# Optimization experiments

Measured on AMD Instinct MI355X. Metric: run time of the kernel, lower is better.

## Reference

```python
import jax, jax.numpy as jnp
import numpy as np

M = 8      # window size
S = 4      # shift size
NH = 3     # num heads
EPS = 1e-5


def _rel_pos_index(m):
    coords = np.stack(np.meshgrid(np.arange(m), np.arange(m), indexing='ij')).reshape(2, -1)
    rel = (coords[:, :, None] - coords[:, None, :]).transpose(1, 2, 0)
    rel[:, :, 0] += m - 1
    rel[:, :, 1] += m - 1
    rel[:, :, 0] *= 2 * m - 1
    return rel.sum(-1)  # [m^2, m^2]


def _attn_mask(Hs, Ws, m, s):
    img = np.zeros((Hs, Ws))
    cnt = 0
    for hsl in (slice(0, -m), slice(-m, -s), slice(-s, None)):
        for wsl in (slice(0, -m), slice(-m, -s), slice(-s, None)):
            img[hsl, wsl] = cnt
            cnt += 1
    mw = img.reshape(Hs // m, m, Ws // m, m).transpose(0, 2, 1, 3).reshape(-1, m * m)
    d = mw[:, None, :] - mw[:, :, None]
    return np.where(d != 0, -100.0, 0.0).astype(np.float32)  # [nW, N, N]


def _ln(x, w, b):
    mu = jnp.mean(x, -1, keepdims=True)
    var = jnp.mean(jnp.square(x - mu), -1, keepdims=True)
    return (x - mu) * jax.lax.rsqrt(var + EPS) * w + b


def setup_inputs() -> dict:
    key = jax.random.key(0)
    ks = jax.random.split(key, 8)
    B, Hs, Ws, C = 16, 128, 128, 96
    MLPH = 4 * C
    inp = {
        'x': jax.random.normal(ks[0], (B, Hs * Ws, C), jnp.float32),
        'norm1_w': jnp.ones((C,), jnp.float32),
        'norm1_b': jnp.zeros((C,), jnp.float32),
        'qkv_w': jax.random.normal(ks[1], (C, 3 * C), jnp.float32) * 0.02,
        'qkv_b': jnp.zeros((3 * C,), jnp.float32),
        'rpb_table': jax.random.normal(ks[2], ((2 * M - 1) ** 2, NH), jnp.float32) * 0.02,
        'proj_w': jax.random.normal(ks[3], (C, C), jnp.float32) * 0.02,
        'proj_b': jnp.zeros((C,), jnp.float32),
        'norm2_w': jnp.ones((C,), jnp.float32),
        'norm2_b': jnp.zeros((C,), jnp.float32),
        'mlp_w1': jax.random.normal(ks[4], (C, MLPH), jnp.float32) * 0.02,
        'mlp_b1': jnp.zeros((MLPH,), jnp.float32),
        'mlp_w2': jax.random.normal(ks[5], (MLPH, C), jnp.float32) * 0.02,
        'mlp_b2': jnp.zeros((C,), jnp.float32),
        'H': Hs,
        'W': Ws,
    }
    return inp


def reference(x, norm1_w, norm1_b, qkv_w, qkv_b, rpb_table, proj_w, proj_b,
              norm2_w, norm2_b, mlp_w1, mlp_b1, mlp_w2, mlp_b2, H, W):
    B, L, C = x.shape
    N = M * M
    HD = C // NH
    scale = HD ** -0.5
    nW = (H // M) * (W // M)

    rpi = jnp.asarray(_rel_pos_index(M))                    # [N, N]
    mask = jnp.asarray(_attn_mask(H, W, M, S))              # [nW, N, N]

    shortcut = x
    h = _ln(x, norm1_w, norm1_b).reshape(B, H, W, C)
    h = jnp.roll(h, (-S, -S), axis=(1, 2))
    # window partition -> [B, nW, N, C]
    h = h.reshape(B, H // M, M, W // M, M, C).transpose(0, 1, 3, 2, 4, 5)
    h = h.reshape(B, nW, N, C)

    qkv = (h @ qkv_w + qkv_b).reshape(B, nW, N, 3, NH, HD)
    q, k, v = qkv[..., 0, :, :], qkv[..., 1, :, :], qkv[..., 2, :, :]  # [B,nW,N,NH,HD]
    attn = jnp.einsum('bwnhd,bwmhd->bwhnm', q, k) * scale              # [B,nW,NH,N,N]
    rp_bias = rpb_table[rpi].transpose(2, 0, 1)                        # [NH,N,N]
    attn = attn + rp_bias[None, None] + mask[None, :, None]
    attn = jax.nn.softmax(attn, axis=-1)
    out = jnp.einsum('bwhnm,bwmhd->bwnhd', attn, v).reshape(B, nW, N, C)
    out = out @ proj_w + proj_b

    # window reverse -> [B, H, W, C]
    out = out.reshape(B, H // M, W // M, M, M, C).transpose(0, 1, 3, 2, 4, 5)
    out = out.reshape(B, H, W, C)
    out = jnp.roll(out, (S, S), axis=(1, 2)).reshape(B, L, C)

    x1 = shortcut + out
    h2 = _ln(x1, norm2_w, norm2_b)
    h2 = jax.nn.gelu(h2 @ mlp_w1 + mlp_b1, approximate=False) @ mlp_w2 + mlp_b2
    return x1 + h2
```

## Files before the change

### kernel.cpp

```cpp
#include <hip/hip_runtime.h>
#include <hip/hip_bf16.h>

typedef __hip_bfloat16 hbf16;
typedef __bf16 bf16_t;
typedef __bf16 bf16x4 __attribute__((ext_vector_type(4)));
typedef __bf16 bf16x8 __attribute__((ext_vector_type(8)));
typedef float  f32x4  __attribute__((ext_vector_type(4)));

__device__ __forceinline__ float b2f(hbf16 v) { return __bfloat162float(v); }

template<bool F32>
__device__ __forceinline__ float ld(const void* p, size_t i) {
    return F32 ? ((const float*)p)[i] : b2f(((const hbf16*)p)[i]);
}

constexpr int Hh  = 128, Ww = 128, Cc = 96;
constexpr int MM  = 8, SS = 4, NHh = 3, C3 = 288;
constexpr int MLPH = 384;
constexpr int NWH = Hh / MM;
constexpr int NW  = NWH * NWH;
constexpr float SCALE = 0.17677669529663687f;
constexpr float EPSf  = 1e-5f;

constexpr int WQKV_ELEMS = C3 * Cc;
constexpr int WP_ELEMS   = Cc * Cc;
constexpr int W1_ELEMS   = MLPH * Cc;
constexpr int W2_ELEMS   = Cc * MLPH;
constexpr int W_TOTAL    = WQKV_ELEMS + WP_ELEMS + W1_ELEMS + W2_ELEMS;

constexpr int OFF_A   = 0;
constexpr int OFF_KA  = 6144;
constexpr int OFF_VT  = 12288;
constexpr int SMEM_E  = 18432;

__global__ void prep_w(const void* __restrict__ qkvw, const void* __restrict__ pw,
                       const void* __restrict__ w1,   const void* __restrict__ w2,
                       const void* __restrict__ n1w,  bf16_t* __restrict__ ws)
{
    const bool f32 = (((const unsigned*)n1w)[0] == 0x3F800000u);
    int i = blockIdx.x * 256 + threadIdx.x;
    if (i < WQKV_ELEMS) {
        int j = i / Cc, k = i - j * Cc;
        ws[i] = (bf16_t)(f32 ? ((const float*)qkvw)[(size_t)k * C3 + j]
                             : b2f(((const hbf16*)qkvw)[(size_t)k * C3 + j]));
    } else if (i < WQKV_ELEMS + WP_ELEMS) {
        int t = i - WQKV_ELEMS;
        int n = t / Cc, r0 = t - n * Cc;
        int p = r0 >> 5, r2 = r0 & 31;
        int quad = r2 >> 3, ii = r2 & 7;
        int k = p * 32 + ((ii >> 2) << 4) + quad * 4 + (ii & 3);
        ws[i] = (bf16_t)(f32 ? ((const float*)pw)[(size_t)k * Cc + n]
                             : b2f(((const hbf16*)pw)[(size_t)k * Cc + n]));
    } else if (i < WQKV_ELEMS + WP_ELEMS + W1_ELEMS) {
        int t = i - WQKV_ELEMS - WP_ELEMS;
        int j = t / Cc, k = t - j * Cc;
        ws[i] = (bf16_t)(f32 ? ((const float*)w1)[(size_t)k * MLPH + j]
                             : b2f(((const hbf16*)w1)[(size_t)k * MLPH + j]));
    } else if (i < W_TOTAL) {
        int t = i - WQKV_ELEMS - WP_ELEMS - W1_ELEMS;
        int n = t / MLPH, r0 = t - n * MLPH;
        int p = r0 >> 5, r2 = r0 & 31;
        int quad = r2 >> 3, ii = r2 & 7;
        int k = p * 32 + ((ii >> 2) << 4) + quad * 4 + (ii & 3);
        ws[i] = (bf16_t)(f32 ? ((const float*)w2)[(size_t)k * Cc + n]
                             : b2f(((const hbf16*)w2)[(size_t)k * Cc + n]));
    }
}

template<bool F32>
__device__ __forceinline__ void swin_body(
    bf16_t* __restrict__ sm,
    const void* __restrict__ x,
    const void* __restrict__ n1w, const void* __restrict__ n1b,
    const void* __restrict__ qkvb, const void* __restrict__ rpb,
    const void* __restrict__ pb,
    const void* __restrict__ n2w, const void* __restrict__ n2b,
    const void* __restrict__ b1,  const void* __restrict__ b2,
    const bf16_t* __restrict__ wq_t, const bf16_t* __restrict__ wp_f,
    const bf16_t* __restrict__ w1_t, const bf16_t* __restrict__ w2_f,
    float* __restrict__ out)
{
    const int tid  = threadIdx.x;
    const int lane = tid & 63;
    const int wv   = tid >> 6;
    const int c16  = lane & 15;
    const int quad = lane >> 4;
    const int b    = blockIdx.x / NW;
    const int w    = blockIdx.x % NW;
    const int wi   = w / NWH, wj = w % NWH;

    {
        const int t = tid >> 2, q = tid & 3;
        const int ri = wi * MM + (t >> 3), rj = wj * MM + (t & 7);
        const int gi = (ri + SS) & (Hh - 1), gj = (rj + SS) & (Ww - 1);
        const size_t base = ((size_t)((b * Hh + gi) * Ww + gj)) * Cc + q * 24;
        float v[24]; float s = 0.f, s2 = 0.f;
        if (F32) {
            const float* xf = (const float*)x + base;
            #pragma unroll
            for (int i = 0; i < 6; ++i) {
                float4 t4 = *(const float4*)(xf + i * 4);
                v[i*4+0] = t4.x; v[i*4+1] = t4.y; v[i*4+2] = t4.z; v[i*4+3] = t4.w;
            }
        } else {
            #pragma unroll
            for (int i = 0; i < 24; ++i) v[i] = b2f(((const hbf16*)x)[base + i]);
        }
        #pragma unroll
        for (int i = 0; i < 24; ++i) { s += v[i]; s2 += v[i] * v[i]; }
        s  += __shfl_xor(s, 1);  s  += __shfl_xor(s, 2);
        s2 += __shfl_xor(s2, 1); s2 += __shfl_xor(s2, 2);
        const float mu = s / Cc, var = s2 / Cc - mu * mu, rstd = rsqrtf(var + EPSf);
        #pragma unroll
        for (int ch = 0; ch < 3; ++ch) {
            float wv8[8], bv8[8];
            if (F32) {
                const float* wf = (const float*)n1w + q * 24 + ch * 8;
                const float* bf = (const float*)n1b + q * 24 + ch * 8;
                float4 w0 = *(const float4*)wf, w1q = *(const float4*)(wf + 4);
                float4 b0 = *(const float4*)bf, b1q = *(const float4*)(bf + 4);
                wv8[0]=w0.x; wv8[1]=w0.y; wv8[2]=w0.z; wv8[3]=w0.w;
                wv8[4]=w1q.x; wv8[5]=w1q.y; wv8[6]=w1q.z; wv8[7]=w1q.w;
                bv8[0]=b0.x; bv8[1]=b0.y; bv8[2]=b0.z; bv8[3]=b0.w;
                bv8[4]=b1q.x; bv8[5]=b1q.y; bv8[6]=b1q.z; bv8[7]=b1q.w;
            } else {
                #pragma unroll
                for (int i = 0; i < 8; ++i) {
                    int cidx = q * 24 + ch * 8 + i;
                    wv8[i] = b2f(((const hbf16*)n1w)[cidx]);
                    bv8[i] = b2f(((const hbf16*)n1b)[cidx]);
                }
            }
            bf16x8 pk;
            #pragma unroll
            for (int i = 0; i < 8; ++i)
                pk[i] = (bf16_t)((v[ch * 8 + i] - mu) * rstd * wv8[i] + bv8[i]);
            *(bf16x8*)&sm[OFF_A + ((q * 3 + ch) * 64 + t) * 8] = pk;
        }
    }

    {
        bf16x8 ha[3];
        #pragma unroll
        for (int ks = 0; ks < 3; ++ks)
            ha[ks] = *(const bf16x8*)&sm[OFF_A + ((ks * 4 + quad) * 64 + wv * 16 + c16) * 8];
        for (int nt = 0; nt < 18; ++nt) {
            const int j = nt * 16 + c16;
            const bf16_t* wrow = wq_t + (size_t)j * Cc + quad * 8;
            f32x4 acc = {0.f, 0.f, 0.f, 0.f};
            acc = __builtin_amdgcn_mfma_f32_16x16x32_bf16(ha[0], *(const bf16x8*)(wrow),      acc, 0, 0, 0);
            acc = __builtin_amdgcn_mfma_f32_16x16x32_bf16(ha[1], *(const bf16x8*)(wrow + 32), acc, 0, 0, 0);
            acc = __builtin_amdgcn_mfma_f32_16x16x32_bf16(ha[2], *(const bf16x8*)(wrow + 64), acc, 0, 0, 0);
            const float bias = ld<F32>(qkvb, j);
            #pragma unroll
            for (int r = 0; r < 4; ++r) {
                const int m = wv * 16 + quad * 4 + r;
                const bf16_t vb = (bf16_t)(acc[r] + bias);
                if (j < 96) {
                    int hd = j >> 5, d = j & 31;
                    sm[OFF_A + ((hd * 4 + (d >> 3)) * 64 + m) * 8 + (d & 7)] = vb;
                } else if (j < 192) {
                    int jj = j - 96; int hd = jj >> 5, d = jj & 31;
                    sm[OFF_KA + ((hd * 4 + (d >> 3)) * 64 + m) * 8 + (d & 7)] = vb;
                } else {
                    int jj = j - 192; int hd = jj >> 5, d = jj & 31;
                    sm[OFF_VT + ((hd * 8 + (m >> 3)) * 32 + d) * 8 + (m & 7)] = vb;
                }
            }
        }
    }
    __syncthreads();

    const int qt_tok = wv * 16 + c16;
    const int qi = qt_tok >> 3, qj = qt_tok & 7;
    bf16x8 ofrag[3];
    {
        const int rq = wi * MM + qi, cq = wj * MM + qj;
        const int regq = (rq < Hh - MM ? 0 : (rq < Hh - SS ? 1 : 2)) * 3
                       + (cq < Ww - MM ? 0 : (cq < Ww - SS ? 1 : 2));
        unsigned rp2[8];
        unsigned penmask = 0;
        #pragma unroll
        for (int nt = 0; nt < 4; ++nt)
            #pragma unroll
            for (int r = 0; r < 4; ++r) {
                const int idx = nt * 4 + r;
                const int k = nt * 16 + quad * 4 + r;
                const int ki = k >> 3, kj = k & 7;
                const int rk = wi * MM + ki, ck = wj * MM + kj;
                const int regk = (rk < Hh - MM ? 0 : (rk < Hh - SS ? 1 : 2)) * 3
                               + (ck < Ww - MM ? 0 : (ck < Ww - SS ? 1 : 2));
                const unsigned rpi = (unsigned)(((qi - ki + 7) * 15 + (qj - kj + 7)) * NHh);
                if (idx & 1) rp2[idx >> 1] |= rpi << 16;
                else         rp2[idx >> 1]  = rpi;
                if (regq != regk) penmask |= 1u << idx;
            }

        #pragma unroll
        for (int hd = 0; hd < NHh; ++hd) {
            bf16x8 qa = *(const bf16x8*)&sm[OFF_A + ((hd * 4 + quad) * 64 + qt_tok) * 8];
            f32x4 sacc[4];
            #pragma unroll
            for (int nt = 0; nt < 4; ++nt) {
                bf16x8 kb = *(const bf16x8*)&sm[OFF_KA + ((hd * 4 + quad) * 64 + nt * 16 + c16) * 8];
                f32x4 z = {0.f, 0.f, 0.f, 0.f};
                sacc[nt] = __builtin_amdgcn_mfma_f32_16x16x32_bf16(kb, qa, z, 0, 0, 0);
            }
            #pragma unroll
            for (int nt = 0; nt < 4; ++nt)
                #pragma unroll
                for (int r = 0; r < 4; ++r) {
                    const int idx = nt * 4 + r;
                    const int rpi = (int)((rp2[idx >> 1] >> ((idx & 1) * 16)) & 0xFFFFu);
                    float sv = sacc[nt][r] * SCALE + ld<F32>(rpb, (size_t)(rpi + hd));
                    if (penmask & (1u << idx)) sv -= 100.0f;
                    sacc[nt][r] = sv;
                }
            f32x4 m4 = sacc[0];
            #pragma unroll
            for (int nt = 1; nt < 4; ++nt)
                #pragma unroll
                for (int r = 0; r < 4; ++r) m4[r] = fmaxf(m4[r], sacc[nt][r]);
            float mx = fmaxf(fmaxf(m4[0], m4[1]), fmaxf(m4[2], m4[3]));
            mx = fmaxf(mx, __shfl_xor(mx, 16));
            mx = fmaxf(mx, __shfl_xor(mx, 32));
            float s = 0.f;
            #pragma unroll
            for (int nt = 0; nt < 4; ++nt)
                #pragma unroll
                for (int r = 0; r < 4; ++r) {
                    float e = __expf(sacc[nt][r] - mx);
                    sacc[nt][r] = e; s += e;
                }
            s += __shfl_xor(s, 16);
            s += __shfl_xor(s, 32);
            const float inv = 1.0f / s;
            bf16x8 pb01, pb23;
            #pragma unroll
            for (int r = 0; r < 4; ++r) {
                pb01[r]     = (bf16_t)(sacc[0][r] * inv);
                pb01[4 + r] = (bf16_t)(sacc[1][r] * inv);
                pb23[r]     = (bf16_t)(sacc[2][r] * inv);
                pb23[4 + r] = (bf16_t)(sacc[3][r] * inv);
            }
            const int g2 = quad >> 1, o2 = (quad & 1) * 4;
            #pragma unroll
            for (int ct = 0; ct < 2; ++ct) {
                const int d = ct * 16 + c16;
                const int vb0 = OFF_VT + ((hd * 8 + g2) * 32 + d) * 8 + o2;
                bf16x4 v0 = *(const bf16x4*)&sm[vb0];
                bf16x4 v1 = *(const bf16x4*)&sm[vb0 + 512];
                bf16x4 v2 = *(const bf16x4*)&sm[vb0 + 1024];
                bf16x4 v3 = *(const bf16x4*)&sm[vb0 + 1536];
                bf16x8 va01, va23;
                #pragma unroll
                for (int i = 0; i < 4; ++i) {
                    va01[i] = v0[i]; va01[4 + i] = v1[i];
                    va23[i] = v2[i]; va23[4 + i] = v3[i];
                }
                f32x4 acc = {0.f, 0.f, 0.f, 0.f};
                acc = __builtin_amdgcn_mfma_f32_16x16x32_bf16(va01, pb01, acc, 0, 0, 0);
                acc = __builtin_amdgcn_mfma_f32_16x16x32_bf16(va23, pb23, acc, 0, 0, 0);
                const int tc = hd * 2 + ct;
                #pragma unroll
                for (int r = 0; r < 4; ++r)
                    ofrag[tc >> 1][(tc & 1) * 4 + r] = (bf16_t)acc[r];
            }
        }
    }

    int gbase[4];
    #pragma unroll
    for (int r = 0; r < 4; ++r) {
        const int m = wv * 16 + quad * 4 + r;
        const int ri = wi * MM + (m >> 3), rj = wj * MM + (m & 7);
        const int gi = (ri + SS) & (Hh - 1), gj = (rj + SS) & (Ww - 1);
        gbase[r] = ((b * Hh + gi) * Ww + gj) * Cc;
    }

    float x1r[24];
    #pragma unroll
    for (int nt = 0; nt < 6; ++nt) {
        const int n = nt * 16 + c16;
        const bf16_t* wr = wp_f + (size_t)n * Cc + quad * 8;
        f32x4 acc = {0.f, 0.f, 0.f, 0.f};
        #pragma unroll
        for (int p = 0; p < 3; ++p)
            acc = __builtin_amdgcn_mfma_f32_16x16x32_bf16(ofrag[p], *(const bf16x8*)(wr + p * 32), acc, 0, 0, 0);
        const float bias = ld<F32>(pb, n);
        #pragma unroll
        for (int r = 0; r < 4; ++r)
            x1r[nt * 4 + r] = ld<F32>(x, (size_t)(gbase[r] + n)) + acc[r] + bias;
    }

    float mu_[4], rs_[4];
    #pragma unroll
    for (int r = 0; r < 4; ++r) {
        float s = 0.f, s2 = 0.f;
        #pragma unroll
        for (int nt = 0; nt < 6; ++nt) { float v = x1r[nt * 4 + r]; s += v; s2 += v * v; }
        s  += __shfl_xor(s, 1);  s  += __shfl_xor(s, 2);  s  += __shfl_xor(s, 4);  s  += __shfl_xor(s, 8);
        s2 += __shfl_xor(s2, 1); s2 += __shfl_xor(s2, 2); s2 += __shfl_xor(s2, 4); s2 += __shfl_xor(s2, 8);
        float mu = s / Cc, var = s2 / Cc - mu * mu;
        mu_[r] = mu; rs_[r] = rsqrtf(var + EPSf);
    }
    #pragma unroll
    for (int nt = 0; nt < 6; ++nt) {
        const int c = nt * 16 + c16;
        const float wc = ld<F32>(n2w, c), bc = ld<F32>(n2b, c);
        #pragma unroll
        for (int r = 0; r < 4; ++r) {
            const int m = wv * 16 + quad * 4 + r;
            sm[OFF_A + ((c >> 3) * 64 + m) * 8 + (c & 7)] =
                (bf16_t)((x1r[nt * 4 + r] - mu_[r]) * rs_[r] * wc + bc);
        }
    }

    {
        bf16x8 h2a[3];
        #pragma unroll
        for (int ks = 0; ks < 3; ++ks)
            h2a[ks] = *(const bf16x8*)&sm[OFF_A + ((ks * 4 + quad) * 64 + wv * 16 + c16) * 8];

        f32x4 acc2[6];
        #pragma unroll
        for (int nt2 = 0; nt2 < 6; ++nt2) acc2[nt2] = {0.f, 0.f, 0.f, 0.f};

        #pragma unroll
        for (int ck = 0; ck < 2; ++ck) {
            bf16x8 hfrag[6];
            #pragma unroll
            for (int jl = 0; jl < 12; ++jl) {
                const int jt = ck * 12 + jl;
                const bf16_t* wrow = w1_t + (size_t)(jt * 16 + c16) * Cc + quad * 8;
                f32x4 acc = {0.f, 0.f, 0.f, 0.f};
                acc = __builtin_amdgcn_mfma_f32_16x16x32_bf16(*(const bf16x8*)(wrow),      h2a[0], acc, 0, 0, 0);
                acc = __builtin_amdgcn_mfma_f32_16x16x32_bf16(*(const bf16x8*)(wrow + 32), h2a[1], acc, 0, 0, 0);
                acc = __builtin_amdgcn_mfma_f32_16x16x32_bf16(*(const bf16x8*)(wrow + 64), h2a[2], acc, 0, 0, 0);
                const int j0 = jt * 16 + quad * 4;
                float bj[4];
                if (F32) {
                    float4 b4 = *(const float4*)((const float*)b1 + j0);
                    bj[0] = b4.x; bj[1] = b4.y; bj[2] = b4.z; bj[3] = b4.w;
                } else {
                    #pragma unroll
                    for (int r = 0; r < 4; ++r) bj[r] = b2f(((const hbf16*)b1)[j0 + r]);
                }
                #pragma unroll
                for (int r = 0; r < 4; ++r) {
                    float a = acc[r] + bj[r];
                    float yn = -2.3022351f * a * (1.0f + 0.044715f * a * a);
                    float g = a / (1.0f + exp2f(yn));
                    hfrag[jl >> 1][(jl & 1) * 4 + r] = (bf16_t)g;
                }
            }
            #pragma unroll
            for (int nt2 = 0; nt2 < 6; ++nt2) {
                const int n = nt2 * 16 + c16;
                const bf16_t* wr = w2_f + (size_t)n * MLPH + (ck * 6) * 32 + quad * 8;
                #pragma unroll
                for (int p = 0; p < 6; ++p)
                    acc2[nt2] = __builtin_amdgcn_mfma_f32_16x16x32_bf16(hfrag[p], *(const bf16x8*)(wr + p * 32), acc2[nt2], 0, 0, 0);
            }
        }

        #pragma unroll
        for (int nt2 = 0; nt2 < 6; ++nt2) {
            const int n = nt2 * 16 + c16;
            const float bn = ld<F32>(b2, n);
            #pragma unroll
            for (int r = 0; r < 4; ++r)
                out[gbase[r] + n] = x1r[nt2 * 4 + r] + acc2[nt2][r] + bn;
        }
    }
}

__global__ __attribute__((amdgpu_flat_work_group_size(256, 256), amdgpu_waves_per_eu(2, 4)))
void swin_fused(const void* __restrict__ x,
                const void* __restrict__ n1w, const void* __restrict__ n1b,
                const void* __restrict__ qkvb, const void* __restrict__ rpb,
                const void* __restrict__ pb,
                const void* __restrict__ n2w, const void* __restrict__ n2b,
                const void* __restrict__ b1,  const void* __restrict__ b2,
                const bf16_t* __restrict__ wq_t, const bf16_t* __restrict__ wp_f,
                const bf16_t* __restrict__ w1_t, const bf16_t* __restrict__ w2_f,
                float* __restrict__ out)
{
    __shared__ __align__(16) bf16_t sm[SMEM_E];
    const bool f32 = (((const unsigned*)n1w)[0] == 0x3F800000u);
    if (f32)
        swin_body<true>(sm, x, n1w, n1b, qkvb, rpb, pb, n2w, n2b, b1, b2,
                        wq_t, wp_f, w1_t, w2_f, out);
    else
        swin_body<false>(sm, x, n1w, n1b, qkvb, rpb, pb, n2w, n2b, b1, b2,
                         wq_t, wp_f, w1_t, w2_f, out);
}

extern "C" void kernel_launch(void* const* d_in, const int* in_sizes, int n_in,
                              void* d_out, int out_size, void* d_ws, size_t ws_size,
                              hipStream_t stream)
{
    const void* x    = d_in[0];
    const void* n1w  = d_in[1];
    const void* n1b  = d_in[2];
    const void* qkvw = d_in[3];
    const void* qkvb = d_in[4];
    const void* rpb  = d_in[5];
    const void* pw   = d_in[6];
    const void* pb   = d_in[7];
    const void* n2w  = d_in[8];
    const void* n2b  = d_in[9];
    const void* w1   = d_in[10];
    const void* b1   = d_in[11];
    const void* w2   = d_in[12];
    const void* b2   = d_in[13];

    const int B = in_sizes[0] / (Hh * Ww * Cc);
    float* out = (float*)d_out;
    bf16_t* wq_t = (bf16_t*)d_ws;
    bf16_t* wp_f = wq_t + WQKV_ELEMS;
    bf16_t* w1_t = wp_f + WP_ELEMS;
    bf16_t* w2_f = w1_t + W1_ELEMS;

    prep_w<<<(W_TOTAL + 255) / 256, 256, 0, stream>>>(qkvw, pw, w1, w2, n1w, wq_t);

    swin_fused<<<B * NW, 256, 0, stream>>>(x, n1w, n1b, qkvb, rpb, pb,
                                           n2w, n2b, b1, b2,
                                           wq_t, wp_f, w1_t, w2_f, out);
}
```

Baseline: 539.7 us.

## Keep Q in registers, transpose QKV GEMM, shrink LDS to raise occupancy

Result: faster. 479.6 us (-11.1%).

```diff
diff --git a/kernel.cpp b/kernel.cpp
--- a/kernel.cpp
+++ b/kernel.cpp
@@ -28,10 +28,9 @@
 constexpr int W2_ELEMS   = Cc * MLPH;
 constexpr int W_TOTAL    = WQKV_ELEMS + WP_ELEMS + W1_ELEMS + W2_ELEMS;
 
-constexpr int OFF_A   = 0;
-constexpr int OFF_KA  = 6144;
-constexpr int OFF_VT  = 12288;
-constexpr int SMEM_E  = 18432;
+constexpr int OFF_AK  = 0;
+constexpr int OFF_V   = 6144;
+constexpr int SMEM_E  = 12288;
 
 __global__ void prep_w(const void* __restrict__ qkvw, const void* __restrict__ pw,
                        const void* __restrict__ w1,   const void* __restrict__ w2,
@@ -88,6 +87,7 @@
     const int b    = blockIdx.x / NW;
     const int w    = blockIdx.x % NW;
     const int wi   = w / NWH, wj = w % NWH;
+    const int my_tok = wv * 16 + c16;
 
     {
         const int t = tid >> 2, q = tid & 3;
@@ -135,44 +135,57 @@
             #pragma unroll
             for (int i = 0; i < 8; ++i)
                 pk[i] = (bf16_t)((v[ch * 8 + i] - mu) * rstd * wv8[i] + bv8[i]);
-            *(bf16x8*)&sm[OFF_A + ((q * 3 + ch) * 64 + t) * 8] = pk;
-        }
-    }
-
+            *(bf16x8*)&sm[OFF_AK + ((q * 3 + ch) * 64 + t) * 8] = pk;
+        }
+    }
+
+    bf16x8 qfrag[3];
     {
         bf16x8 ha[3];
         #pragma unroll
         for (int ks = 0; ks < 3; ++ks)
-            ha[ks] = *(const bf16x8*)&sm[OFF_A + ((ks * 4 + quad) * 64 + wv * 16 + c16) * 8];
+            ha[ks] = *(const bf16x8*)&sm[OFF_AK + ((ks * 4 + quad) * 64 + my_tok) * 8];
+
+        #pragma unroll
         for (int nt = 0; nt < 18; ++nt) {
-            const int j = nt * 16 + c16;
-            const bf16_t* wrow = wq_t + (size_t)j * Cc + quad * 8;
+            const bf16_t* wrow = wq_t + (size_t)(nt * 16 + c16) * Cc + quad * 8;
             f32x4 acc = {0.f, 0.f, 0.f, 0.f};
-            acc = __builtin_amdgcn_mfma_f32_16x16x32_bf16(ha[0], *(const bf16x8*)(wrow),      acc, 0, 0, 0);
-            acc = __builtin_amdgcn_mfma_f32_16x16x32_bf16(ha[1], *(const bf16x8*)(wrow + 32), acc, 0, 0, 0);
-            acc = __builtin_amdgcn_mfma_f32_16x16x32_bf16(ha[2], *(const bf16x8*)(wrow + 64), acc, 0, 0, 0);
-            const float bias = ld<F32>(qkvb, j);
-            #pragma unroll
-            for (int r = 0; r < 4; ++r) {
-                const int m = wv * 16 + quad * 4 + r;
-                const bf16_t vb = (bf16_t)(acc[r] + bias);
-                if (j < 96) {
-                    int hd = j >> 5, d = j & 31;
-                    sm[OFF_A + ((hd * 4 + (d >> 3)) * 64 + m) * 8 + (d & 7)] = vb;
-                } else if (j < 192) {
-                    int jj = j - 96; int hd = jj >> 5, d = jj & 31;
-                    sm[OFF_KA + ((hd * 4 + (d >> 3)) * 64 + m) * 8 + (d & 7)] = vb;
-                } else {
-                    int jj = j - 192; int hd = jj >> 5, d = jj & 31;
-                    sm[OFF_VT + ((hd * 8 + (m >> 3)) * 32 + d) * 8 + (m & 7)] = vb;
+            acc = __builtin_amdgcn_mfma_f32_16x16x32_bf16(*(const bf16x8*)(wrow),      ha[0], acc, 0, 0, 0);
+            acc = __builtin_amdgcn_mfma_f32_16x16x32_bf16(*(const bf16x8*)(wrow + 32), ha[1], acc, 0, 0, 0);
+            acc = __builtin_amdgcn_mfma_f32_16x16x32_bf16(*(const bf16x8*)(wrow + 64), ha[2], acc, 0, 0, 0);
+            const int j0 = nt * 16 + quad * 4;
+            float bj[4];
+            if (F32) {
+                float4 b4 = *(const float4*)((const float*)qkvb + j0);
+                bj[0] = b4.x; bj[1] = b4.y; bj[2] = b4.z; bj[3] = b4.w;
+            } else {
+                #pragma unroll
+                for (int r = 0; r < 4; ++r) bj[r] = b2f(((const hbf16*)qkvb)[j0 + r]);
+            }
+            bf16x4 ov;
+            #pragma unroll
+            for (int r = 0; r < 4; ++r) ov[r] = (bf16_t)(acc[r] + bj[r]);
+
+            if (nt < 6) {
+                const int hd = nt >> 1, ct = nt & 1;
+                #pragma unroll
+                for (int r = 0; r < 4; ++r) qfrag[hd][ct * 4 + r] = ov[r];
+            } else if (nt < 12) {
+                const int kk = nt - 6, hd = kk >> 1, ct = kk & 1;
+                *(bf16x4*)&sm[OFF_AK + ((hd * 4 + quad) * 64 + my_tok) * 8 + ct * 4] = ov;
+            } else {
+                const int dv = (nt - 12) * 16 + quad * 4;
+                #pragma unroll
+                for (int r = 0; r < 4; ++r) {
+                    const int d = dv + r, hd = d >> 5, dd = d & 31;
+                    sm[OFF_V + ((hd * 8 + (my_tok >> 3)) * 32 + dd) * 8 + (my_tok & 7)] = ov[r];
                 }
             }
         }
     }
     __syncthreads();
 
-    const int qt_tok = wv * 16 + c16;
-    const int qi = qt_tok >> 3, qj = qt_tok & 7;
+    const int qi = my_tok >> 3, qj = my_tok & 7;
     bf16x8 ofrag[3];
     {
         const int rq = wi * MM + qi, cq = wj * MM + qj;
@@ -198,13 +211,12 @@
 
         #pragma unroll
         for (int hd = 0; hd < NHh; ++hd) {
-            bf16x8 qa = *(const bf16x8*)&sm[OFF_A + ((hd * 4 + quad) * 64 + qt_tok) * 8];
             f32x4 sacc[4];
             #pragma unroll
             for (int nt = 0; nt < 4; ++nt) {
-                bf16x8 kb = *(const bf16x8*)&sm[OFF_KA + ((hd * 4 + quad) * 64 + nt * 16 + c16) * 8];
+                bf16x8 kb = *(const bf16x8*)&sm[OFF_AK + ((hd * 4 + quad) * 64 + nt * 16 + c16) * 8];
                 f32x4 z = {0.f, 0.f, 0.f, 0.f};
-                sacc[nt] = __builtin_amdgcn_mfma_f32_16x16x32_bf16(kb, qa, z, 0, 0, 0);
+                sacc[nt] = __builtin_amdgcn_mfma_f32_16x16x32_bf16(kb, qfrag[hd], z, 0, 0, 0);
             }
             #pragma unroll
             for (int nt = 0; nt < 4; ++nt)
@@ -247,7 +259,7 @@
             #pragma unroll
             for (int ct = 0; ct < 2; ++ct) {
                 const int d = ct * 16 + c16;
-                const int vb0 = OFF_VT + ((hd * 8 + g2) * 32 + d) * 8 + o2;
+                const int vb0 = OFF_V + ((hd * 8 + g2) * 32 + d) * 8 + o2;
                 bf16x4 v0 = *(const bf16x4*)&sm[vb0];
                 bf16x4 v1 = *(const bf16x4*)&sm[vb0 + 512];
                 bf16x4 v2 = *(const bf16x4*)&sm[vb0 + 1024];
@@ -304,6 +316,9 @@
         float mu = s / Cc, var = s2 / Cc - mu * mu;
         mu_[r] = mu; rs_[r] = rsqrtf(var + EPSf);
     }
+
+    __syncthreads();
+
     #pragma unroll
     for (int nt = 0; nt < 6; ++nt) {
         const int c = nt * 16 + c16;
@@ -311,7 +326,7 @@
         #pragma unroll
         for (int r = 0; r < 4; ++r) {
             const int m = wv * 16 + quad * 4 + r;
-            sm[OFF_A + ((c >> 3) * 64 + m) * 8 + (c & 7)] =
+            sm[OFF_AK + ((c >> 3) * 64 + m) * 8 + (c & 7)] =
                 (bf16_t)((x1r[nt * 4 + r] - mu_[r]) * rs_[r] * wc + bc);
         }
     }
@@ -320,11 +335,16 @@
         bf16x8 h2a[3];
         #pragma unroll
         for (int ks = 0; ks < 3; ++ks)
-            h2a[ks] = *(const bf16x8*)&sm[OFF_A + ((ks * 4 + quad) * 64 + wv * 16 + c16) * 8];
+            h2a[ks] = *(const bf16x8*)&sm[OFF_AK + ((ks * 4 + quad) * 64 + my_tok) * 8];
 
         f32x4 acc2[6];
         #pragma unroll
-        for (int nt2 = 0; nt2 < 6; ++nt2) acc2[nt2] = {0.f, 0.f, 0.f, 0.f};
+        for (int nt2 = 0; nt2 < 6; ++nt2) {
+            const int n = nt2 * 16 + c16;
+            const float bn = ld<F32>(b2, n);
+            #pragma unroll
+            for (int r = 0; r < 4; ++r) acc2[nt2][r] = x1r[nt2 * 4 + r] + bn;
+        }
 
         #pragma unroll
         for (int ck = 0; ck < 2; ++ck) {
@@ -367,15 +387,14 @@
         #pragma unroll
         for (int nt2 = 0; nt2 < 6; ++nt2) {
             const int n = nt2 * 16 + c16;
-            const float bn = ld<F32>(b2, n);
             #pragma unroll
             for (int r = 0; r < 4; ++r)
-                out[gbase[r] + n] = x1r[nt2 * 4 + r] + acc2[nt2][r] + bn;
+                out[gbase[r] + n] = acc2[nt2][r];
         }
     }
 }
 
-__global__ __attribute__((amdgpu_flat_work_group_size(256, 256), amdgpu_waves_per_eu(2, 4)))
+__global__ __attribute__((amdgpu_flat_work_group_size(256, 256), amdgpu_waves_per_eu(2, 6)))
 void swin_fused(const void* __restrict__ x,
                 const void* __restrict__ n1w, const void* __restrict__ n1b,
                 const void* __restrict__ qkvb, const void* __restrict__ rpb,
```
